# Kernel tuning notes

Measured on AMD Instinct MI355X. Metric: run time of the kernel, lower is better.

The kernel has to match this reference:

```python
import jax, jax.numpy as jnp
import numpy as np

N_NODES = 50000
N_EDGES = 800000
D = 128
N_LAYERS = 5
N_REL = 500
N_ENT = 50000  # fc output size (num_entities)
BATCH = 1024


def setup_inputs() -> dict:
    key = jax.random.key(0)
    ks = jax.random.split(key, 10)
    return {
        "entity_embed": jax.random.normal(ks[0], (N_NODES, D), dtype=jnp.float32),
        "edge_val": jnp.ones((N_EDGES,), dtype=jnp.float32),
        "gnn_W": jax.random.normal(ks[1], (N_LAYERS, D, D), dtype=jnp.float32) * (1.0 / np.sqrt(D)),
        "gnn_b": jax.random.normal(ks[2], (N_LAYERS, D), dtype=jnp.float32) * 0.01,
        "rel_table": jax.random.normal(ks[3], (N_REL, D), dtype=jnp.float32),
        "fc_W": jax.random.normal(ks[4], (2 * D, N_ENT), dtype=jnp.float32) * (1.0 / np.sqrt(2 * D)),
        "fc_b": jax.random.normal(ks[5], (N_ENT,), dtype=jnp.float32) * 0.01,
        "edge_row": jax.random.randint(ks[6], (N_EDGES,), 0, N_NODES, dtype=jnp.int32),
        "edge_col": jax.random.randint(ks[7], (N_EDGES,), 0, N_NODES, dtype=jnp.int32),
        "head_idx": jax.random.randint(ks[8], (BATCH,), 0, N_NODES, dtype=jnp.int32),
        "rel_ids": jax.random.randint(ks[9], (BATCH,), 0, N_REL, dtype=jnp.int32),
    }


def reference(entity_embed, edge_val, gnn_W, gnn_b, rel_table, fc_W, fc_b,
              edge_row, edge_col, head_idx, rel_ids):
    n_nodes = entity_embed.shape[0]

    def layer(x, wb):
        W, b = wb
        # sparse.mm(adj, x): out[row] += val * x[col]
        msgs = edge_val[:, None] * x[edge_col]          # [E, D]
        agg = jax.ops.segment_sum(msgs, edge_row, num_segments=n_nodes)  # [N, D]
        return jax.nn.relu(agg @ W + b), None

    all_embed, _ = jax.lax.scan(layer, entity_embed, (gnn_W, gnn_b))

    head_embed = all_embed[head_idx]                    # [B, D]
    rel_embed = rel_table[rel_ids]                      # [B, D]
    embed = jnp.concatenate([head_embed, rel_embed], axis=1)  # [B, 2D]
    logits = embed @ fc_W + fc_b                        # [B, N_ENT]
    return logits
```

## Files before the change

### kernel.cpp

```cpp
#include <hip/hip_runtime.h>


#define N_NODES 50000
#define N_EDGES 800000
#define D 128
#define N_LAYERS 5
#define N_ENT 50000
#define BATCH 1024
#define KDIM 256
#define SCAN_BLOCKS ((N_NODES + 255) / 256)
#define FC_NT 128

#define CVT_A_BLOCKS 3125
#define CVT_B_BLOCKS 320
#define CVT_C_BLOCKS 6250

typedef __attribute__((ext_vector_type(8))) __bf16 bf16x8;
typedef __attribute__((ext_vector_type(4))) float f32x4;
typedef __attribute__((ext_vector_type(8))) unsigned short u16x8;
typedef __attribute__((ext_vector_type(4))) unsigned short u16x4;

__device__ inline unsigned short f2bf(float x) {
  unsigned int u = __float_as_uint(x);
  unsigned int r = (u + 0x7FFFu + ((u >> 16) & 1u)) >> 16;
  return (unsigned short)r;
}
__device__ inline float bf2f(unsigned short b) {
  return __uint_as_float(((unsigned int)b) << 16);
}

__global__ void zero_i32(int* __restrict__ p, int n) {
  int i = blockIdx.x * blockDim.x + threadIdx.x;
  if (i < n) p[i] = 0;
}

__global__ void hist_kernel(const int* __restrict__ rows, int* __restrict__ counts) {
  int i = blockIdx.x * blockDim.x + threadIdx.x;
  int stride = gridDim.x * blockDim.x;
  for (; i < N_EDGES; i += stride) atomicAdd(&counts[rows[i]], 1);
}

__device__ inline int block_exscan256(int v, int* wsum, int* tot) {
  int t = threadIdx.x, lane = t & 63, wid = t >> 6;
  int s = v;
#pragma unroll
  for (int off = 1; off < 64; off <<= 1) {
    int u = __shfl_up(s, off, 64);
    if (lane >= off) s += u;
  }
  if (lane == 63) wsum[wid] = s;
  __syncthreads();
  if (t == 0) {
    int run = 0;
#pragma unroll
    for (int w = 0; w < 4; ++w) { int tmp = wsum[w]; wsum[w] = run; run += tmp; }
    wsum[4] = run;
  }
  __syncthreads();
  *tot = wsum[4];
  return wsum[wid] + s - v;
}

__global__ __launch_bounds__(256) void scan1_kernel(const int* __restrict__ counts,
                                                    int* __restrict__ row_ptr,
                                                    int* __restrict__ bsum) {
  __shared__ int wsum[5];
  int i = blockIdx.x * 256 + threadIdx.x;
  int v = (i < N_NODES) ? counts[i] : 0;
  int tot;
  int ex = block_exscan256(v, wsum, &tot);
  if (i < N_NODES) row_ptr[i] = ex;
  if (threadIdx.x == 0) bsum[blockIdx.x] = tot;
}

__global__ __launch_bounds__(256) void scan2_kernel(int* __restrict__ bsum) {
  __shared__ int wsum[5];
  int t = threadIdx.x;
  int v = (t < SCAN_BLOCKS) ? bsum[t] : 0;
  int tot;
  int ex = block_exscan256(v, wsum, &tot);
  if (t < SCAN_BLOCKS) bsum[t] = ex;
}

__global__ __launch_bounds__(256) void scan3_kernel(const int* __restrict__ counts,
                                                    const int* __restrict__ bsum,
                                                    int* __restrict__ row_ptr,
                                                    int* __restrict__ cursor) {
  int i = blockIdx.x * 256 + threadIdx.x;
  if (i >= N_NODES) return;
  int ex = row_ptr[i] + bsum[blockIdx.x];
  row_ptr[i] = ex;
  cursor[i] = ex;
  if (i == N_NODES - 1) row_ptr[N_NODES] = ex + counts[i];
}

__global__ void scatter_kernel(const int* __restrict__ rows, const int* __restrict__ cols,
                               const float* __restrict__ vals, int* __restrict__ cursor,
                               int* __restrict__ col_s, float* __restrict__ val_s) {
  int i = blockIdx.x * blockDim.x + threadIdx.x;
  int stride = gridDim.x * blockDim.x;
  for (; i < N_EDGES; i += stride) {
    int r = rows[i];
    int pos = atomicAdd(&cursor[r], 1);
    col_s[pos] = cols[i];
    val_s[pos] = vals[i];
  }
}

__global__ __launch_bounds__(256) void convert_all(const float* __restrict__ entity,
                                                   const float* __restrict__ gW,
                                                   const float* __restrict__ fcW,
                                                   unsigned short* __restrict__ entbf,
                                                   unsigned short* __restrict__ Wt5,
                                                   unsigned short* __restrict__ Wt) {
  int bid = blockIdx.x;
  int t = threadIdx.x;
  if (bid < CVT_A_BLOCKS) {
    int i = bid * 256 + t;
    float4 a = *(const float4*)&entity[i * 8];
    float4 b = *(const float4*)&entity[i * 8 + 4];
    u16x8 o;
    o[0] = f2bf(a.x); o[1] = f2bf(a.y); o[2] = f2bf(a.z); o[3] = f2bf(a.w);
    o[4] = f2bf(b.x); o[5] = f2bf(b.y); o[6] = f2bf(b.z); o[7] = f2bf(b.w);
    *(u16x8*)&entbf[i * 8] = o;
  } else if (bid < CVT_A_BLOCKS + CVT_B_BLOCKS) {
    int idx = (bid - CVT_A_BLOCKS) * 256 + t;
    int l = idx / (D * D);
    int rem = idx - l * D * D;
    int j = rem >> 7;
    int k = rem & 127;
    Wt5[idx] = f2bf(gW[l * D * D + k * D + j]);
  } else {
    int id = (bid - CVT_A_BLOCKS - CVT_B_BLOCKS) * 256 + t;
    int kg = id / N_ENT;
    int n = id - kg * N_ENT;
    int k0 = kg * 8;
    u16x8 pk;
#pragma unroll
    for (int e = 0; e < 8; ++e) pk[e] = f2bf(fcW[(size_t)(k0 + e) * N_ENT + n]);
    *(u16x8*)&Wt[(size_t)n * KDIM + k0] = pk;
  }
}

__device__ inline void agg_batch(int cl, float vl, int cnt, int q, int l16,
                                 const unsigned short* __restrict__ xb, float* acc) {
  int j = 0;
  for (; j + 4 <= cnt; j += 4) {
    int c[4]; float v[4]; u16x8 xv[4];
#pragma unroll
    for (int u = 0; u < 4; ++u) {
      c[u] = __shfl(cl, q * 16 + j + u);
      v[u] = __shfl(vl, q * 16 + j + u);
    }
#pragma unroll
    for (int u = 0; u < 4; ++u) xv[u] = *(const u16x8*)&xb[c[u] * D + l16 * 8];
#pragma unroll
    for (int u = 0; u < 4; ++u)
#pragma unroll
      for (int dd = 0; dd < 8; ++dd) acc[dd] = fmaf(v[u], bf2f(xv[u][dd]), acc[dd]);
  }
  for (; j < cnt; ++j) {
    int c = __shfl(cl, q * 16 + j);
    float v = __shfl(vl, q * 16 + j);
    u16x8 xv0 = *(const u16x8*)&xb[c * D + l16 * 8];
#pragma unroll
    for (int dd = 0; dd < 8; ++dd) acc[dd] = fmaf(v, bf2f(xv0[dd]), acc[dd]);
  }
}

__global__ __launch_bounds__(256) void layer_fused(const unsigned short* __restrict__ xb,
                                                   const int* __restrict__ row_ptr,
                                                   const int* __restrict__ cols,
                                                   const float* __restrict__ vals,
                                                   const unsigned short* __restrict__ Bt,
                                                   const float* __restrict__ bias,
                                                   unsigned short* __restrict__ yb) {
  __shared__ unsigned short atile[64 * D];
  int t = threadIdx.x, lane = t & 63, wave = t >> 6;
  int q = lane >> 4, l16 = lane & 15;
  int r0 = blockIdx.x * 64;
  char* ab = (char*)atile;

#pragma unroll
  for (int p = 0; p < 4; ++p) {
    int row_l = wave * 16 + p * 4 + q;
    int r = r0 + row_l;
    float acc[8] = {0.f, 0.f, 0.f, 0.f, 0.f, 0.f, 0.f, 0.f};
    if (r < N_NODES) {
      int e0 = row_ptr[r], e1 = row_ptr[r + 1];
      for (int base = e0; base < e1; base += 16) {
        int idx = base + l16;
        bool ok = idx < e1;
        int cl = ok ? cols[idx] : 0;
        float vl = ok ? vals[idx] : 0.f;
        agg_batch(cl, vl, min(16, e1 - base), q, l16, xb, acc);
      }
    }
    u16x8 o;
#pragma unroll
    for (int dd = 0; dd < 8; ++dd) o[dd] = f2bf(acc[dd]);
    *(u16x8*)(ab + row_l * 256 + ((l16 ^ (row_l & 7)) << 4)) = o;
  }
  __syncthreads();

  int lq = lane >> 4;
  f32x4 acc2[4][2];
#pragma unroll
  for (int m = 0; m < 4; ++m) { acc2[m][0] = (f32x4){0,0,0,0}; acc2[m][1] = (f32x4){0,0,0,0}; }
#pragma unroll
  for (int kk = 0; kk < 4; ++kk) {
    bf16x8 wfr[2];
#pragma unroll
    for (int nt = 0; nt < 2; ++nt)
      wfr[nt] = *(const bf16x8*)&Bt[(wave * 32 + nt * 16 + l16) * D + kk * 32 + lq * 8];
#pragma unroll
    for (int m = 0; m < 4; ++m) {
      int row_l = m * 16 + l16;
      bf16x8 afr = *(const bf16x8*)(ab + row_l * 256 + ((((kk * 4 + lq) ^ (row_l & 7)) << 4)));
      acc2[m][0] = __builtin_amdgcn_mfma_f32_16x16x32_bf16(wfr[0], afr, acc2[m][0], 0, 0, 0);
      acc2[m][1] = __builtin_amdgcn_mfma_f32_16x16x32_bf16(wfr[1], afr, acc2[m][1], 0, 0, 0);
    }
  }
#pragma unroll
  for (int nt = 0; nt < 2; ++nt) {
    int jb = wave * 32 + nt * 16 + lq * 4;
    float4 bb = *(const float4*)&bias[jb];
#pragma unroll
    for (int m = 0; m < 4; ++m) {
      int r = r0 + m * 16 + l16;
      if (r < N_NODES) {
        u16x4 o;
        o[0] = f2bf(fmaxf(acc2[m][nt][0] + bb.x, 0.f));
        o[1] = f2bf(fmaxf(acc2[m][nt][1] + bb.y, 0.f));
        o[2] = f2bf(fmaxf(acc2[m][nt][2] + bb.z, 0.f));
        o[3] = f2bf(fmaxf(acc2[m][nt][3] + bb.w, 0.f));
        *(u16x4*)&yb[(size_t)r * D + jb] = o;
      }
    }
  }
}

__global__ __launch_bounds__(256) void layer_head(const unsigned short* __restrict__ xb,
                                                  const int* __restrict__ row_ptr,
                                                  const int* __restrict__ cols,
                                                  const float* __restrict__ vals,
                                                  const int* __restrict__ head_idx,
                                                  const float* __restrict__ rel_table,
                                                  const int* __restrict__ rel_ids,
                                                  const unsigned short* __restrict__ Bt,
                                                  const float* __restrict__ bias,
                                                  unsigned short* __restrict__ ebf) {
  __shared__ unsigned short atile[64 * D];
  int t = threadIdx.x, lane = t & 63, wave = t >> 6;
  int q = lane >> 4, l16 = lane & 15;
  int r0 = blockIdx.x * 64;
  char* ab = (char*)atile;

#pragma unroll
  for (int it = 0; it < 4; ++it) {
    int c = it * 256 + t;
    int bl = c >> 4;
    int kq = c & 15;
    int b = r0 + bl;
    const float* rp = &rel_table[(size_t)rel_ids[b] * D + kq * 8];
    float4 a0 = *(const float4*)rp;
    float4 a1 = *(const float4*)(rp + 4);
    u16x8 o;
    o[0] = f2bf(a0.x); o[1] = f2bf(a0.y); o[2] = f2bf(a0.z); o[3] = f2bf(a0.w);
    o[4] = f2bf(a1.x); o[5] = f2bf(a1.y); o[6] = f2bf(a1.z); o[7] = f2bf(a1.w);
    *(u16x8*)&ebf[(size_t)b * KDIM + D + kq * 8] = o;
  }

#pragma unroll
  for (int p = 0; p < 4; ++p) {
    int row_l = wave * 16 + p * 4 + q;
    int b = r0 + row_l;
    int r = head_idx[b];
    float acc[8] = {0.f, 0.f, 0.f, 0.f, 0.f, 0.f, 0.f, 0.f};
    int e0 = row_ptr[r], e1 = row_ptr[r + 1];
    for (int base = e0; base < e1; base += 16) {
      int idx = base + l16;
      bool ok = idx < e1;
      int cl = ok ? cols[idx] : 0;
      float vl = ok ? vals[idx] : 0.f;
      agg_batch(cl, vl, min(16, e1 - base), q, l16, xb, acc);
    }
    u16x8 o;
#pragma unroll
    for (int dd = 0; dd < 8; ++dd) o[dd] = f2bf(acc[dd]);
    *(u16x8*)(ab + row_l * 256 + ((l16 ^ (row_l & 7)) << 4)) = o;
  }
  __syncthreads();

  int lq = lane >> 4;
  f32x4 acc2[4][2];
#pragma unroll
  for (int m = 0; m < 4; ++m) { acc2[m][0] = (f32x4){0,0,0,0}; acc2[m][1] = (f32x4){0,0,0,0}; }
#pragma unroll
  for (int kk = 0; kk < 4; ++kk) {
    bf16x8 wfr[2];
#pragma unroll
    for (int nt = 0; nt < 2; ++nt)
      wfr[nt] = *(const bf16x8*)&Bt[(wave * 32 + nt * 16 + l16) * D + kk * 32 + lq * 8];
#pragma unroll
    for (int m = 0; m < 4; ++m) {
      int row_l = m * 16 + l16;
      bf16x8 afr = *(const bf16x8*)(ab + row_l * 256 + ((((kk * 4 + lq) ^ (row_l & 7)) << 4)));
      acc2[m][0] = __builtin_amdgcn_mfma_f32_16x16x32_bf16(wfr[0], afr, acc2[m][0], 0, 0, 0);
      acc2[m][1] = __builtin_amdgcn_mfma_f32_16x16x32_bf16(wfr[1], afr, acc2[m][1], 0, 0, 0);
    }
  }
#pragma unroll
  for (int nt = 0; nt < 2; ++nt) {
    int jb = wave * 32 + nt * 16 + lq * 4;
    float4 bb = *(const float4*)&bias[jb];
#pragma unroll
    for (int m = 0; m < 4; ++m) {
      int b = r0 + m * 16 + l16;
      u16x4 o;
      o[0] = f2bf(fmaxf(acc2[m][nt][0] + bb.x, 0.f));
      o[1] = f2bf(fmaxf(acc2[m][nt][1] + bb.y, 0.f));
      o[2] = f2bf(fmaxf(acc2[m][nt][2] + bb.z, 0.f));
      o[3] = f2bf(fmaxf(acc2[m][nt][3] + bb.w, 0.f));
      *(u16x4*)&ebf[(size_t)b * KDIM + jb] = o;
    }
  }
}

__global__ __launch_bounds__(256, 2) void fc_mfma(const unsigned short* __restrict__ ebf,
                                                  const unsigned short* __restrict__ Wt,
                                                  const float* __restrict__ fcb,
                                                  float* __restrict__ out) {
  __shared__ unsigned short etile[64 * KDIM];
  int t = threadIdx.x;
  int lane = t & 63, wave = t >> 6;
  int l16 = lane & 15, lq = lane >> 4;
  int n0 = blockIdx.x * FC_NT;
  char* eb = (char*)etile;

  bf16x8 afr[2][8];
#pragma unroll
  for (int nt = 0; nt < 2; ++nt) {
    const unsigned short* wp = Wt + (size_t)(n0 + wave * 32 + nt * 16 + l16) * KDIM + lq * 8;
#pragma unroll
    for (int kk = 0; kk < 8; ++kk) afr[nt][kk] = *(const bf16x8*)(wp + kk * 32);
  }

  int n_st[2]; float4 bv[2];
#pragma unroll
  for (int nt = 0; nt < 2; ++nt) {
    n_st[nt] = n0 + wave * 32 + nt * 16 + lq * 4;
    bv[nt] = make_float4(0.f, 0.f, 0.f, 0.f);
    if (n_st[nt] < N_ENT) bv[nt] = *(const float4*)&fcb[n_st[nt]];
  }

  for (int bc = 0; bc < 8; ++bc) {
    int b0 = blockIdx.y * 512 + bc * 64;
    const char* esrc = (const char*)(ebf + (size_t)b0 * KDIM);
#pragma unroll
    for (int it = 0; it < 8; ++it) {
      int c = it * 256 + t;
      int row = c >> 5;
      int ci = c & 31;
      float4 v = *(const float4*)(esrc + (size_t)c * 16);
      *(float4*)(eb + row * 512 + ((ci ^ ((row & 7) << 2)) << 4)) = v;
    }
    __syncthreads();

    f32x4 acc[2][4];
#pragma unroll
    for (int nt = 0; nt < 2; ++nt)
#pragma unroll
      for (int m = 0; m < 4; ++m) acc[nt][m] = (f32x4){0.f, 0.f, 0.f, 0.f};

#pragma unroll
    for (int m = 0; m < 4; ++m) {
      int row = m * 16 + l16;
#pragma unroll
      for (int kk = 0; kk < 8; ++kk) {
        bf16x8 bfr = *(const bf16x8*)(eb + row * 512 + ((((kk * 4 + lq) ^ ((row & 7) << 2)) << 4)));
        acc[0][m] = __builtin_amdgcn_mfma_f32_16x16x32_bf16(afr[0][kk], bfr, acc[0][m], 0, 0, 0);
        acc[1][m] = __builtin_amdgcn_mfma_f32_16x16x32_bf16(afr[1][kk], bfr, acc[1][m], 0, 0, 0);
      }
    }

#pragma unroll
    for (int nt = 0; nt < 2; ++nt) {
      if (n_st[nt] < N_ENT) {
#pragma unroll
        for (int m = 0; m < 4; ++m) {
          int b = b0 + m * 16 + l16;
          float4 o = {acc[nt][m][0] + bv[nt].x, acc[nt][m][1] + bv[nt].y,
                      acc[nt][m][2] + bv[nt].z, acc[nt][m][3] + bv[nt].w};
          *(float4*)&out[(size_t)b * N_ENT + n_st[nt]] = o;
        }
      }
    }
    __syncthreads();
  }
}

extern "C" void kernel_launch(void* const* d_in, const int* in_sizes, int n_in,
                              void* d_out, int out_size, void* d_ws, size_t ws_size,
                              hipStream_t stream) {
  const float* entity    = (const float*)d_in[0];
  const float* edge_val  = (const float*)d_in[1];
  const float* gnn_W     = (const float*)d_in[2];
  const float* gnn_b     = (const float*)d_in[3];
  const float* rel_table = (const float*)d_in[4];
  const float* fc_W      = (const float*)d_in[5];
  const float* fc_b      = (const float*)d_in[6];
  const int* edge_row    = (const int*)d_in[7];
  const int* edge_col    = (const int*)d_in[8];
  const int* head_idx    = (const int*)d_in[9];
  const int* rel_ids     = (const int*)d_in[10];
  float* out = (float*)d_out;

  char* ws = (char*)d_ws;
  size_t off = 0;
  auto alloc = [&](size_t bytes) -> void* {
    void* p = ws + off;
    off = (off + bytes + 255) & ~(size_t)255;
    return p;
  };
  int* counts   = (int*)alloc((size_t)N_NODES * 4);
  int* row_ptr  = (int*)alloc((size_t)(N_NODES + 1) * 4);
  int* cursor   = (int*)alloc((size_t)N_NODES * 4);
  int* bsum     = (int*)alloc((size_t)256 * 4);
  int* col_s    = (int*)alloc((size_t)N_EDGES * 4);
  float* val_s  = (float*)alloc((size_t)N_EDGES * 4);
  unsigned short* xA    = (unsigned short*)alloc((size_t)N_NODES * D * 2);
  unsigned short* xB    = (unsigned short*)alloc((size_t)N_NODES * D * 2);
  unsigned short* entbf = (unsigned short*)alloc((size_t)N_NODES * D * 2);
  unsigned short* ebf   = (unsigned short*)alloc((size_t)BATCH * KDIM * 2);
  unsigned short* Wt    = (unsigned short*)alloc((size_t)(N_ENT + 256) * KDIM * 2);
  unsigned short* Wt5   = (unsigned short*)alloc((size_t)N_LAYERS * D * D * 2);

  zero_i32<<<(N_NODES + 255) / 256, 256, 0, stream>>>(counts, N_NODES);
  hist_kernel<<<1024, 256, 0, stream>>>(edge_row, counts);
  scan1_kernel<<<SCAN_BLOCKS, 256, 0, stream>>>(counts, row_ptr, bsum);
  scan2_kernel<<<1, 256, 0, stream>>>(bsum);
  scan3_kernel<<<SCAN_BLOCKS, 256, 0, stream>>>(counts, bsum, row_ptr, cursor);
  scatter_kernel<<<1024, 256, 0, stream>>>(edge_row, edge_col, edge_val, cursor, col_s, val_s);

  convert_all<<<CVT_A_BLOCKS + CVT_B_BLOCKS + CVT_C_BLOCKS, 256, 0, stream>>>(
      entity, gnn_W, fc_W, entbf, Wt5, Wt);

  for (int layer = 0; layer < N_LAYERS - 1; ++layer) {
    const unsigned short* xin = (layer == 0) ? entbf : ((layer & 1) ? xA : xB);
    unsigned short* yout = (layer & 1) ? xB : xA;
    layer_fused<<<(N_NODES + 63) / 64, 256, 0, stream>>>(xin, row_ptr, col_s, val_s,
                                                         Wt5 + (size_t)layer * D * D,
                                                         gnn_b + (size_t)layer * D, yout);
  }

  layer_head<<<BATCH / 64, 256, 0, stream>>>(xB, row_ptr, col_s, val_s, head_idx,
                                             rel_table, rel_ids,
                                             Wt5 + (size_t)(N_LAYERS - 1) * D * D,
                                             gnn_b + (size_t)(N_LAYERS - 1) * D, ebf);

  dim3 fcg((N_ENT + FC_NT - 1) / FC_NT, 2);
  fc_mfma<<<fcg, 256, 0, stream>>>(ebf, Wt, fc_b, out);
}
```

Measured before the change: 378.4 us.

## Fuse CSR construction kernels into one cooperative kernel with grid syncs

Replaces the six separate CSR-building launches (zero, histogram, three scan stages, scatter) with a single cooperative kernel that uses grid-wide barriers between phases. The goal is to cut per-launch overhead and the idle gaps between small kernels. In exchange it adds five grid.sync barriers, and it relies on all 1024 blocks being co-resident. If the cooperative launch fails, nothing else in the code detects it.

```diff
diff --git a/kernel.cpp b/kernel.cpp
--- a/kernel.cpp
+++ b/kernel.cpp
@@ -1,4 +1,7 @@
 #include <hip/hip_runtime.h>
+#include <hip/hip_cooperative_groups.h>
+
+namespace cg = cooperative_groups;
 
 
 #define N_NODES 50000
@@ -10,6 +13,7 @@
 #define KDIM 256
 #define SCAN_BLOCKS ((N_NODES + 255) / 256)
 #define FC_NT 128
+#define CSR_GRID 1024
 
 #define CVT_A_BLOCKS 3125
 #define CVT_B_BLOCKS 320
@@ -29,17 +33,6 @@
   return __uint_as_float(((unsigned int)b) << 16);
 }
 
-__global__ void zero_i32(int* __restrict__ p, int n) {
-  int i = blockIdx.x * blockDim.x + threadIdx.x;
-  if (i < n) p[i] = 0;
-}
-
-__global__ void hist_kernel(const int* __restrict__ rows, int* __restrict__ counts) {
-  int i = blockIdx.x * blockDim.x + threadIdx.x;
-  int stride = gridDim.x * blockDim.x;
-  for (; i < N_EDGES; i += stride) atomicAdd(&counts[rows[i]], 1);
-}
-
 __device__ inline int block_exscan256(int v, int* wsum, int* tot) {
   int t = threadIdx.x, lane = t & 63, wid = t >> 6;
   int s = v;
@@ -61,49 +54,61 @@
   return wsum[wid] + s - v;
 }
 
-__global__ __launch_bounds__(256) void scan1_kernel(const int* __restrict__ counts,
-                                                    int* __restrict__ row_ptr,
-                                                    int* __restrict__ bsum) {
-  __shared__ int wsum[5];
-  int i = blockIdx.x * 256 + threadIdx.x;
-  int v = (i < N_NODES) ? counts[i] : 0;
-  int tot;
-  int ex = block_exscan256(v, wsum, &tot);
-  if (i < N_NODES) row_ptr[i] = ex;
-  if (threadIdx.x == 0) bsum[blockIdx.x] = tot;
-}
-
-__global__ __launch_bounds__(256) void scan2_kernel(int* __restrict__ bsum) {
+__global__ __launch_bounds__(256) void csr_build(const int* __restrict__ edge_row,
+                                                 const int* __restrict__ edge_col,
+                                                 const float* __restrict__ edge_val,
+                                                 int* __restrict__ counts,
+                                                 int* __restrict__ row_ptr,
+                                                 int* __restrict__ cursor,
+                                                 int* __restrict__ bsum,
+                                                 int* __restrict__ col_s,
+                                                 float* __restrict__ val_s) {
+  cg::grid_group grid = cg::this_grid();
   __shared__ int wsum[5];
   int t = threadIdx.x;
-  int v = (t < SCAN_BLOCKS) ? bsum[t] : 0;
-  int tot;
-  int ex = block_exscan256(v, wsum, &tot);
-  if (t < SCAN_BLOCKS) bsum[t] = ex;
-}
-
-__global__ __launch_bounds__(256) void scan3_kernel(const int* __restrict__ counts,
-                                                    const int* __restrict__ bsum,
-                                                    int* __restrict__ row_ptr,
-                                                    int* __restrict__ cursor) {
-  int i = blockIdx.x * 256 + threadIdx.x;
-  if (i >= N_NODES) return;
-  int ex = row_ptr[i] + bsum[blockIdx.x];
-  row_ptr[i] = ex;
-  cursor[i] = ex;
-  if (i == N_NODES - 1) row_ptr[N_NODES] = ex + counts[i];
-}
-
-__global__ void scatter_kernel(const int* __restrict__ rows, const int* __restrict__ cols,
-                               const float* __restrict__ vals, int* __restrict__ cursor,
-                               int* __restrict__ col_s, float* __restrict__ val_s) {
-  int i = blockIdx.x * blockDim.x + threadIdx.x;
-  int stride = gridDim.x * blockDim.x;
-  for (; i < N_EDGES; i += stride) {
-    int r = rows[i];
+  int gid = blockIdx.x * 256 + t;
+  int gstride = gridDim.x * 256;
+
+  for (int i = gid; i < N_NODES; i += gstride) counts[i] = 0;
+  grid.sync();
+
+  for (int i = gid; i < N_EDGES; i += gstride) atomicAdd(&counts[edge_row[i]], 1);
+  grid.sync();
+
+  if (blockIdx.x < SCAN_BLOCKS) {
+    int i = blockIdx.x * 256 + t;
+    int v = (i < N_NODES) ? counts[i] : 0;
+    int tot;
+    int ex = block_exscan256(v, wsum, &tot);
+    if (i < N_NODES) row_ptr[i] = ex;
+    if (t == 0) bsum[blockIdx.x] = tot;
+  }
+  grid.sync();
+
+  if (blockIdx.x == 0) {
+    int v = (t < SCAN_BLOCKS) ? bsum[t] : 0;
+    int tot;
+    int ex = block_exscan256(v, wsum, &tot);
+    if (t < SCAN_BLOCKS) bsum[t] = ex;
+  }
+  grid.sync();
+
+  if (blockIdx.x < SCAN_BLOCKS) {
+    int i = blockIdx.x * 256 + t;
+    if (i < N_NODES) {
+      int ex = row_ptr[i] + bsum[blockIdx.x];
+      row_ptr[i] = ex;
+      cursor[i] = ex;
+      if (i == N_NODES - 1) row_ptr[N_NODES] = ex + counts[i];
+    }
+  }
+  grid.sync();
+
+  for (int i = gid; i < N_EDGES; i += gstride) {
+    int r = edge_row[i];
     int pos = atomicAdd(&cursor[r], 1);
-    col_s[pos] = cols[i];
-    val_s[pos] = vals[i];
+    col_s[pos] = edge_col[i];
+    val_s[pos] = edge_val[i];
   }
 }
 
@@ -436,12 +441,13 @@
   unsigned short* Wt    = (unsigned short*)alloc((size_t)(N_ENT + 256) * KDIM * 2);
   unsigned short* Wt5   = (unsigned short*)alloc((size_t)N_LAYERS * D * D * 2);
 
-  zero_i32<<<(N_NODES + 255) / 256, 256, 0, stream>>>(counts, N_NODES);
-  hist_kernel<<<1024, 256, 0, stream>>>(edge_row, counts);
-  scan1_kernel<<<SCAN_BLOCKS, 256, 0, stream>>>(counts, row_ptr, bsum);
-  scan2_kernel<<<1, 256, 0, stream>>>(bsum);
-  scan3_kernel<<<SCAN_BLOCKS, 256, 0, stream>>>(counts, bsum, row_ptr, cursor);
-  scatter_kernel<<<1024, 256, 0, stream>>>(edge_row, edge_col, edge_val, cursor, col_s, val_s);
+  {
+    void* args[] = {(void*)&edge_row, (void*)&edge_col, (void*)&edge_val,
+                    (void*)&counts, (void*)&row_ptr, (void*)&cursor,
+                    (void*)&bsum, (void*)&col_s, (void*)&val_s};
+    hipLaunchCooperativeKernel((const void*)csr_build, dim3(CSR_GRID), dim3(256),
+                               args, 0, stream);
+  }
 
   convert_all<<<CVT_A_BLOCKS + CVT_B_BLOCKS + CVT_C_BLOCKS, 256, 0, stream>>>(
       entity, gnn_W, fc_W, entbf, Wt5, Wt);
```

Result: slower. 841.0 us (+122.3%).
